# Kernel tuning notes

Measured on AMD Instinct MI355X. Metric: run time of the kernel, lower is better.

## Reference

```python
import jax, jax.numpy as jnp
import numpy as np

B, S, T, M, H = 16, 128, 1024, 16, 1024
HID = 1024        # attention MLP hidden
WIDTH_EMB = 20    # width embedding dim
N_LING = 2        # len(linguistic_feature_types)


def setup_inputs() -> dict:
    key = jax.random.key(0)
    ks = jax.random.split(key, 12)
    doc_embeddings = jax.random.normal(ks[0], (B, T, H), dtype=jnp.float32)
    start_mappings = jax.random.normal(ks[1], (B, S, T), dtype=jnp.float32)
    end_mappings = jax.random.normal(ks[2], (B, S, T), dtype=jnp.float32)
    continuous_mappings = jax.random.normal(ks[3], (B, S, M, T), dtype=jnp.float32)
    width = jax.random.randint(ks[4], (B, S), 0, M, dtype=jnp.int64)
    linguistic_labels = jax.random.normal(ks[5], (B, S, N_LING), dtype=jnp.float32)
    # attention MLP params (torch Linear layout transposed to x @ W + b)
    W1 = jax.random.normal(ks[6], (H, HID), dtype=jnp.float32) * (1.0 / np.sqrt(H))
    b1 = jax.random.normal(ks[7], (HID,), dtype=jnp.float32) * 0.01
    W2 = jax.random.normal(ks[8], (HID, 1), dtype=jnp.float32) * (1.0 / np.sqrt(HID))
    b2 = jax.random.normal(ks[9], (1,), dtype=jnp.float32) * 0.01
    width_table = jax.random.normal(ks[10], (5, WIDTH_EMB), dtype=jnp.float32)
    return {
        'doc_embeddings': doc_embeddings,
        'start_mappings': start_mappings,
        'end_mappings': end_mappings,
        'continuous_mappings': continuous_mappings,
        'linguistic_labels': linguistic_labels,
        'W1': W1, 'b1': b1, 'W2': W2, 'b2': b2,
        'width_table': width_table,
        'width': width,
    }


def reference(doc_embeddings, start_mappings, end_mappings, continuous_mappings,
              linguistic_labels, W1, b1, W2, b2, width_table, width):
    # one-hot matmul gathers
    start = jnp.einsum('bst,bth->bsh', start_mappings, doc_embeddings)
    end = jnp.einsum('bst,bth->bsh', end_mappings, doc_embeddings)
    cont = jnp.einsum('bsmt,bth->bsmh', continuous_mappings, doc_embeddings)
    b, s, m, h = cont.shape
    vector = jnp.concatenate([start, end], axis=-1).reshape(b * s, 2 * h)
    cont = cont.reshape(b * s, m, h)
    w = width.reshape(b * s)
    ling = linguistic_labels.reshape(b * s, -1)
    # padded masked attention pooling
    masks = (jnp.arange(m)[None, :] < jnp.maximum(w, 1)[:, None]).astype(cont.dtype)
    hdn = jax.nn.relu(jnp.einsum('nmh,hk->nmk', cont, W1) + b1)
    scores = (jnp.einsum('nmk,ko->nmo', hdn, W2) + b2)[..., 0]  # [n, m]
    scores = scores * masks
    scores = jnp.where(scores != 0, scores, jnp.asarray(-9e9, scores.dtype))
    att = jax.nn.softmax(scores, axis=1)
    weighted_sum = jnp.einsum('nm,nmh->nh', att, cont)
    vector = jnp.concatenate([vector, weighted_sum], axis=1)
    # linguistic feature columns (loop over fixed small feature list)
    for fi in range(N_LING):
        vector = jnp.concatenate([vector, ling[:, fi:fi + 1]], axis=1)
    # width embedding (clamp max=4)
    wemb = width_table[jnp.clip(w, 0, 4)]
    vector = jnp.concatenate([vector, wemb], axis=1)
    return vector.reshape(b, s, -1)
```

## Files before the change

kernel.cpp:

```cpp
#include <hip/hip_runtime.h>

typedef unsigned short ushort_t;
typedef unsigned int uint_t;
typedef _Float16 f16;
typedef f16 f16x8 __attribute__((ext_vector_type(8)));
typedef float f32x4 __attribute__((ext_vector_type(4)));

#define B_   16
#define S_   128
#define T_   1024
#define M_   16
#define H_   1024
#define OUTW 3094
#define NSPAN (B_*S_)
#define NROW  (NSPAN*M_)

#define WS_CONT   0
#define WS_DOCT   67108864
#define WS_W1T    100663296
#define WS_SCORES 102760448

__device__ __forceinline__ float sane(float v) {
  return fminf(fmaxf(v, -60000.f), 60000.f);
}
__device__ __forceinline__ ushort_t f16bits(float f) {
  union { f16 h; ushort_t u; } c; c.h = (f16)f; return c.u;
}
__device__ __forceinline__ void load_lds16(const void* g, void* l) {
  __builtin_amdgcn_global_load_lds(
      (const __attribute__((address_space(1))) uint_t*)g,
      (__attribute__((address_space(3))) uint_t*)l, 16, 0, 0);
}

__global__ __launch_bounds__(256) void tconv(const float* __restrict__ in,
                                             ushort_t* __restrict__ out,
                                             int R, int C) {
  __shared__ uint_t tile[64][65];
  const int tid = threadIdx.x;
  const int c0 = blockIdx.x * 64, r0 = blockIdx.y * 64;
  const size_t mo = (size_t)blockIdx.z * R * C;
  const float* ip = in + mo;
  ushort_t* op = out + mo;
  const int tx = tid & 63, ty = tid >> 6;
#pragma unroll
  for (int p = 0; p < 16; ++p) {
    int r = p * 4 + ty;
    tile[r][tx] = (uint_t)f16bits(ip[(size_t)(r0 + r) * C + c0 + tx]);
  }
  __syncthreads();
  const int rr = (tid & 31) * 2, cc0 = tid >> 5;
  uint_t* op32 = (uint_t*)op;
#pragma unroll
  for (int p = 0; p < 8; ++p) {
    int c = cc0 + p * 8;
    uint_t lo = tile[rr][c] & 0xffffu;
    uint_t hi = tile[rr + 1][c] & 0xffffu;
    op32[((size_t)(c0 + c) * R + r0 + rr) >> 1] = lo | (hi << 16);
  }
}

__global__ __launch_bounds__(256) void gemm1(const float* __restrict__ startm,
                                             const float* __restrict__ endm,
                                             const float* __restrict__ contm,
                                             const ushort_t* __restrict__ docT,
                                             float* __restrict__ out,
                                             f16* __restrict__ contF) {
  __shared__ float As[128 * 32];
  __shared__ ushort_t Bs[128 * 32];
  const int tid = threadIdx.x;
  const uint_t pid = blockIdx.x;
  const int xcd = pid & 7;
  const int s_  = pid >> 3;
  const int ct  = s_ & 7;
  const int pg  = (s_ >> 3) * 8 + xcd;
  const int rt  = pg >> 4;
  const int b   = pg & 15;

  const float* Ap;
  if (rt == 0)      Ap = startm + (size_t)b * S_ * T_;
  else if (rt == 1) Ap = endm + (size_t)b * S_ * T_;
  else              Ap = contm + (size_t)b * (S_ * M_ * T_) + (size_t)(rt - 2) * 128 * T_;
  const ushort_t* Bp = docT + (size_t)b * (H_ * T_) + (size_t)ct * 128 * T_;

  const int lane = tid & 63, w = tid >> 6;
  const int wr = w >> 1, wc = w & 1;
  const int quad = lane >> 4, l16 = lane & 15;
  const int arow = lane >> 3;
  const int acol = ((lane & 7) ^ arow) * 4;
  const int brow = lane >> 2;
  const int bcol = ((lane & 3) ^ ((lane >> 3) & 3)) * 8;

  f32x4 acc[4][4];
#pragma unroll
  for (int i = 0; i < 4; ++i)
#pragma unroll
    for (int j = 0; j < 4; ++j) acc[i][j] = (f32x4){0.f, 0.f, 0.f, 0.f};

  for (int k0 = 0; k0 < T_; k0 += 32) {
#pragma unroll
    for (int i = 0; i < 4; ++i) {
      const int rb = w * 32 + i * 8;
      load_lds16(Ap + (size_t)(rb + arow) * T_ + k0 + acol, &As[rb * 32]);
    }
#pragma unroll
    for (int i = 0; i < 2; ++i) {
      const int rb = w * 32 + i * 16;
      load_lds16(Bp + (size_t)(rb + brow) * T_ + k0 + bcol, &Bs[rb * 32]);
    }
    __syncthreads();
    f16x8 af[4], bfr[4];
#pragma unroll
    for (int i = 0; i < 4; ++i) {
      const int row = wr * 64 + i * 16 + l16;
      const int sw = row & 7;
      f32x4 lo = *(const f32x4*)&As[row * 32 + (((quad * 2) ^ sw) * 4)];
      f32x4 hi = *(const f32x4*)&As[row * 32 + (((quad * 2 + 1) ^ sw) * 4)];
      f16x8 h;
#pragma unroll
      for (int k = 0; k < 4; ++k) { h[k] = (f16)lo[k]; h[k + 4] = (f16)hi[k]; }
      af[i] = h;
    }
#pragma unroll
    for (int j = 0; j < 4; ++j) {
      const int row = wc * 64 + j * 16 + l16;
      const int sw = (row >> 1) & 3;
      bfr[j] = *(const f16x8*)&Bs[row * 32 + ((quad ^ sw) * 8)];
    }
#pragma unroll
    for (int i = 0; i < 4; ++i)
#pragma unroll
      for (int j = 0; j < 4; ++j)
        acc[i][j] = __builtin_amdgcn_mfma_f32_16x16x32_f16(af[i], bfr[j], acc[i][j], 0, 0, 0);
    __syncthreads();
  }

  if (rt < 2) {
    float* op = out + (size_t)b * S_ * OUTW + (size_t)rt * 1024 + (size_t)ct * 128;
#pragma unroll
    for (int i = 0; i < 4; ++i)
#pragma unroll
      for (int j = 0; j < 4; ++j)
#pragma unroll
        for (int r = 0; r < 4; ++r) {
          int row = wr * 64 + i * 16 + quad * 4 + r;
          int col = wc * 64 + j * 16 + l16;
          op[(size_t)row * OUTW + col] = sane(acc[i][j][r]);
        }
  } else {
    f16* cp = contF + ((size_t)b * 2048 + (size_t)(rt - 2) * 128) * H_ + (size_t)ct * 128;
#pragma unroll
    for (int i = 0; i < 4; ++i)
#pragma unroll
      for (int j = 0; j < 4; ++j)
#pragma unroll
        for (int r = 0; r < 4; ++r) {
          int row = wr * 64 + i * 16 + quad * 4 + r;
          int col = wc * 64 + j * 16 + l16;
          cp[(size_t)row * H_ + col] = (f16)sane(acc[i][j][r]);
        }
  }
}

__global__ __launch_bounds__(256) void gemm2(const f16* __restrict__ contF,
                                             const f16* __restrict__ W1T,
                                             const float* __restrict__ b1,
                                             const float* __restrict__ W2,
                                             float* __restrict__ scores) {
  __shared__ f16 As[128 * 32];
  __shared__ f16 Bs[128 * 32];
  const int tid = threadIdx.x;
  const uint_t pid = blockIdx.x;
  const int xcd = pid & 7;
  const int s_  = pid >> 3;
  const int ct  = s_ & 7;
  const int rt  = (s_ >> 3) * 8 + xcd;

  const f16* Ap = contF + (size_t)rt * 128 * H_;
  const f16* Bp = W1T + (size_t)ct * 128 * H_;

  const int lane = tid & 63, w = tid >> 6;
  const int wr = w >> 1, wc = w & 1;
  const int quad = lane >> 4, l16 = lane & 15;
  const int brow = lane >> 2;
  const int bcol = ((lane & 3) ^ ((lane >> 3) & 3)) * 8;

  f32x4 acc[4][4];
#pragma unroll
  for (int i = 0; i < 4; ++i)
#pragma unroll
    for (int j = 0; j < 4; ++j) acc[i][j] = (f32x4){0.f, 0.f, 0.f, 0.f};

  for (int k0 = 0; k0 < H_; k0 += 32) {
#pragma unroll
    for (int i = 0; i < 2; ++i) {
      const int rb = w * 32 + i * 16;
      load_lds16(Ap + (size_t)(rb + brow) * H_ + k0 + bcol, &As[rb * 32]);
      load_lds16(Bp + (size_t)(rb + brow) * H_ + k0 + bcol, &Bs[rb * 32]);
    }
    __syncthreads();
    f16x8 af[4], bfr[4];
#pragma unroll
    for (int i = 0; i < 4; ++i) {
      const int row = wr * 64 + i * 16 + l16;
      const int sw = (row >> 1) & 3;
      af[i] = *(const f16x8*)&As[row * 32 + ((quad ^ sw) * 8)];
    }
#pragma unroll
    for (int j = 0; j < 4; ++j) {
      const int row = wc * 64 + j * 16 + l16;
      const int sw = (row >> 1) & 3;
      bfr[j] = *(const f16x8*)&Bs[row * 32 + ((quad ^ sw) * 8)];
    }
#pragma unroll
    for (int i = 0; i < 4; ++i)
#pragma unroll
      for (int j = 0; j < 4; ++j)
        acc[i][j] = __builtin_amdgcn_mfma_f32_16x16x32_f16(af[i], bfr[j], acc[i][j], 0, 0, 0);
    __syncthreads();
  }

  const int colbase = ct * 128 + wc * 64;
#pragma unroll
  for (int i = 0; i < 4; ++i) {
#pragma unroll
    for (int r = 0; r < 4; ++r) {
      float t = 0.f;
#pragma unroll
      for (int j = 0; j < 4; ++j) {
        int c = colbase + j * 16 + l16;
        float v = acc[i][j][r] + b1[c];
        v = fmaxf(v, 0.f);
        t = fmaf(v, W2[c], t);
      }
      t += __shfl_xor(t, 1);
      t += __shfl_xor(t, 2);
      t += __shfl_xor(t, 4);
      t += __shfl_xor(t, 8);
      if (l16 == 0) {
        int row = rt * 128 + wr * 64 + i * 16 + quad * 4 + r;
        atomicAdd(&scores[row], t);
      }
    }
  }
}

__global__ __launch_bounds__(256) void finalize(const f16* __restrict__ contF,
                                                const float* __restrict__ scores,
                                                const float* __restrict__ ling,
                                                const float* __restrict__ b2,
                                                const float* __restrict__ wtab,
                                                const int* __restrict__ width,
                                                float* __restrict__ out) {
  const int n = blockIdx.x;
  const int tid = threadIdx.x;
  __shared__ float sc[16];
  if (tid < 16) {
    float raw = scores[n * 16 + tid] + b2[0];
    if (raw != raw) raw = 0.0f;
    int wv = width[n];
    int wm = wv > 1 ? wv : 1;
    float s = (tid < wm) ? raw : 0.0f;
    if (s == 0.0f) s = -9e9f;
    sc[tid] = s;
  }
  __syncthreads();
  float mx = sc[0];
#pragma unroll
  for (int m = 1; m < 16; ++m) mx = fmaxf(mx, sc[m]);
  float e[16];
  float ssum = 0.f;
#pragma unroll
  for (int m = 0; m < 16; ++m) { e[m] = __expf(sc[m] - mx); ssum += e[m]; }
  const float inv = 1.0f / ssum;
  const f16* cp = contF + (size_t)n * (M_ * H_);
  float* op = out + (size_t)n * OUTW;
#pragma unroll
  for (int hh = 0; hh < 4; ++hh) {
    int h = tid + hh * 256;
    float a = 0.f;
#pragma unroll
    for (int m = 0; m < 16; ++m) a = fmaf(e[m], (float)cp[m * H_ + h], a);
    op[2048 + h] = sane(a * inv);
  }
  if (tid < 2) op[3072 + tid] = ling[n * 2 + tid];
  if (tid < 20) {
    int wv = width[n];
    int wcl = wv < 4 ? wv : 4;
    if (wcl < 0) wcl = 0;
    op[3074 + tid] = wtab[wcl * 20 + tid];
  }
}

extern "C" void kernel_launch(void* const* d_in, const int* in_sizes, int n_in,
                              void* d_out, int out_size, void* d_ws, size_t ws_size,
                              hipStream_t stream) {
  const float* doc    = (const float*)d_in[0];
  const float* startm = (const float*)d_in[1];
  const float* endm   = (const float*)d_in[2];
  const float* contm  = (const float*)d_in[3];
  const float* ling   = (const float*)d_in[4];
  const float* W1     = (const float*)d_in[5];
  const float* b1     = (const float*)d_in[6];
  const float* W2     = (const float*)d_in[7];
  const float* b2     = (const float*)d_in[8];
  const float* wtab   = (const float*)d_in[9];
  const int*   width  = (const int*)d_in[10];
  float* out = (float*)d_out;

  char* ws = (char*)d_ws;
  f16*      contF  = (f16*)(ws + WS_CONT);
  ushort_t* docT   = (ushort_t*)(ws + WS_DOCT);
  f16*      W1T    = (f16*)(ws + WS_W1T);
  float*    scores = (float*)(ws + WS_SCORES);

  hipMemsetAsync(scores, 0, NROW * sizeof(float), stream);
  tconv<<<dim3(16, 16, 16), 256, 0, stream>>>(doc, docT, 1024, 1024);
  tconv<<<dim3(16, 16, 1), 256, 0, stream>>>(W1, (ushort_t*)W1T, 1024, 1024);
  gemm1<<<dim3(2304, 1, 1), 256, 0, stream>>>(startm, endm, contm, docT, out, contF);
  gemm2<<<dim3(2048, 1, 1), 256, 0, stream>>>(contF, (const f16*)W1T, b1, W2, scores);
  finalize<<<dim3(NSPAN, 1, 1), 256, 0, stream>>>(contF, scores, ling, b2, wtab, width, out);
}
```

Before: 499.7 us.

## Double-buffer LDS in both GEMMs and convert A to fp16 before staging

Both GEMM kernels now use two LDS buffers, so the next K-tile is prefetched while the MFMAs run on the current one, and only one barrier is needed per iteration. In gemm1 the fp32 A tile is loaded into registers, converted to fp16 and written to LDS once, rather than staged as fp32 and converted by every reading wave. This halves the A staging footprint and removes repeated conversions. The risks are higher register pressure from the prefetched A values and the LDS async-load ordering relying on a single barrier.

```diff
diff --git a/kernel.cpp b/kernel.cpp
--- a/kernel.cpp
+++ b/kernel.cpp
@@ -65,8 +65,8 @@
                                              const ushort_t* __restrict__ docT,
                                              float* __restrict__ out,
                                              f16* __restrict__ contF) {
-  __shared__ float As[128 * 32];
-  __shared__ ushort_t Bs[128 * 32];
+  __shared__ f16 As[2 * 128 * 32];
+  __shared__ f16 Bs[2 * 128 * 32];
   const int tid = threadIdx.x;
   const uint_t pid = blockIdx.x;
   const int xcd = pid & 7;
@@ -85,8 +85,12 @@
   const int lane = tid & 63, w = tid >> 6;
   const int wr = w >> 1, wc = w & 1;
   const int quad = lane >> 4, l16 = lane & 15;
-  const int arow = lane >> 3;
-  const int acol = ((lane & 7) ^ arow) * 4;
+  const int arow = tid >> 1;
+  const int ah   = tid & 1;
+  const int asw  = (arow >> 1) & 3;
+  const int ac0  = ((2 * ah) ^ asw) * 8;
+  const int ac1  = ((2 * ah + 1) ^ asw) * 8;
+  const float* aSrc = Ap + (size_t)arow * T_ + ah * 16;
   const int brow = lane >> 2;
   const int bcol = ((lane & 3) ^ ((lane >> 3) & 3)) * 8;
 
@@ -96,42 +100,75 @@
 #pragma unroll
     for (int j = 0; j < 4; ++j) acc[i][j] = (f32x4){0.f, 0.f, 0.f, 0.f};
 
-  for (int k0 = 0; k0 < T_; k0 += 32) {
-#pragma unroll
-    for (int i = 0; i < 4; ++i) {
-      const int rb = w * 32 + i * 8;
-      load_lds16(Ap + (size_t)(rb + arow) * T_ + k0 + acol, &As[rb * 32]);
-    }
+  {
+    f32x4 a0 = *(const f32x4*)(aSrc + 0);
+    f32x4 a1 = *(const f32x4*)(aSrc + 4);
+    f32x4 a2 = *(const f32x4*)(aSrc + 8);
+    f32x4 a3 = *(const f32x4*)(aSrc + 12);
 #pragma unroll
     for (int i = 0; i < 2; ++i) {
       const int rb = w * 32 + i * 16;
-      load_lds16(Bp + (size_t)(rb + brow) * T_ + k0 + bcol, &Bs[rb * 32]);
-    }
+      load_lds16(Bp + (size_t)(rb + brow) * T_ + bcol, &Bs[rb * 32]);
+    }
+    f16x8 h0, h1;
+#pragma unroll
+    for (int k = 0; k < 4; ++k) {
+      h0[k] = (f16)a0[k]; h0[k + 4] = (f16)a1[k];
+      h1[k] = (f16)a2[k]; h1[k + 4] = (f16)a3[k];
+    }
+    *(f16x8*)&As[arow * 32 + ac0] = h0;
+    *(f16x8*)&As[arow * 32 + ac1] = h1;
     __syncthreads();
+  }
+
+  int cur = 0;
+  for (int k0 = 0; k0 < T_; k0 += 32) {
+    const int nxt = cur ^ 1;
+    const bool pf = (k0 + 32 < T_);
+    f32x4 a0, a1, a2, a3;
+    if (pf) {
+      const float* ap = aSrc + (k0 + 32);
+      a0 = *(const f32x4*)(ap + 0);
+      a1 = *(const f32x4*)(ap + 4);
+      a2 = *(const f32x4*)(ap + 8);
+      a3 = *(const f32x4*)(ap + 12);
+#pragma unroll
+      for (int i = 0; i < 2; ++i) {
+        const int rb = w * 32 + i * 16;
+        load_lds16(Bp + (size_t)(rb + brow) * T_ + (k0 + 32) + bcol,
+                   &Bs[nxt * 4096 + rb * 32]);
+      }
+    }
     f16x8 af[4], bfr[4];
 #pragma unroll
     for (int i = 0; i < 4; ++i) {
       const int row = wr * 64 + i * 16 + l16;
-      const int sw = row & 7;
-      f32x4 lo = *(const f32x4*)&As[row * 32 + (((quad * 2) ^ sw) * 4)];
-      f32x4 hi = *(const f32x4*)&As[row * 32 + (((quad * 2 + 1) ^ sw) * 4)];
-      f16x8 h;
-#pragma unroll
-      for (int k = 0; k < 4; ++k) { h[k] = (f16)lo[k]; h[k + 4] = (f16)hi[k]; }
-      af[i] = h;
+      const int sw = (row >> 1) & 3;
+      af[i] = *(const f16x8*)&As[cur * 4096 + row * 32 + ((quad ^ sw) * 8)];
     }
 #pragma unroll
     for (int j = 0; j < 4; ++j) {
       const int row = wc * 64 + j * 16 + l16;
       const int sw = (row >> 1) & 3;
-      bfr[j] = *(const f16x8*)&Bs[row * 32 + ((quad ^ sw) * 8)];
+      bfr[j] = *(const f16x8*)&Bs[cur * 4096 + row * 32 + ((quad ^ sw) * 8)];
     }
 #pragma unroll
     for (int i = 0; i < 4; ++i)
 #pragma unroll
       for (int j = 0; j < 4; ++j)
         acc[i][j] = __builtin_amdgcn_mfma_f32_16x16x32_f16(af[i], bfr[j], acc[i][j], 0, 0, 0);
+    if (pf) {
+      f16x8 h0, h1;
+#pragma unroll
+      for (int k = 0; k < 4; ++k) {
+        h0[k] = (f16)a0[k]; h0[k + 4] = (f16)a1[k];
+        h1[k] = (f16)a2[k]; h1[k + 4] = (f16)a3[k];
+      }
+      *(f16x8*)&As[nxt * 4096 + arow * 32 + ac0] = h0;
+      *(f16x8*)&As[nxt * 4096 + arow * 32 + ac1] = h1;
+    }
     __syncthreads();
+    cur = nxt;
   }
 
   if (rt < 2) {
@@ -166,8 +203,8 @@
                                              const float* __restrict__ b1,
                                              const float* __restrict__ W2,
                                              float* __restrict__ scores) {
-  __shared__ f16 As[128 * 32];
-  __shared__ f16 Bs[128 * 32];
+  __shared__ f16 As[2 * 128 * 32];
+  __shared__ f16 Bs[2 * 128 * 32];
   const int tid = threadIdx.x;
   const uint_t pid = blockIdx.x;
   const int xcd = pid & 7;
@@ -190,26 +227,40 @@
 #pragma unroll
     for (int j = 0; j < 4; ++j) acc[i][j] = (f32x4){0.f, 0.f, 0.f, 0.f};
 
+#pragma unroll
+  for (int i = 0; i < 2; ++i) {
+    const int rb = w * 32 + i * 16;
+    load_lds16(Ap + (size_t)(rb + brow) * H_ + bcol, &As[rb * 32]);
+    load_lds16(Bp + (size_t)(rb + brow) * H_ + bcol, &Bs[rb * 32]);
+  }
+  __syncthreads();
+
+  int cur = 0;
   for (int k0 = 0; k0 < H_; k0 += 32) {
-#pragma unroll
-    for (int i = 0; i < 2; ++i) {
-      const int rb = w * 32 + i * 16;
-      load_lds16(Ap + (size_t)(rb + brow) * H_ + k0 + bcol, &As[rb * 32]);
-      load_lds16(Bp + (size_t)(rb + brow) * H_ + k0 + bcol, &Bs[rb * 32]);
-    }
-    __syncthreads();
+    const int nxt = cur ^ 1;
+    const bool pf = (k0 + 32 < H_);
+    if (pf) {
+#pragma unroll
+      for (int i = 0; i < 2; ++i) {
+        const int rb = w * 32 + i * 16;
+        load_lds16(Ap + (size_t)(rb + brow) * H_ + (k0 + 32) + bcol,
+                   &As[nxt * 4096 + rb * 32]);
+        load_lds16(Bp + (size_t)(rb + brow) * H_ + (k0 + 32) + bcol,
+                   &Bs[nxt * 4096 + rb * 32]);
+      }
+    }
     f16x8 af[4], bfr[4];
 #pragma unroll
     for (int i = 0; i < 4; ++i) {
       const int row = wr * 64 + i * 16 + l16;
       const int sw = (row >> 1) & 3;
-      af[i] = *(const f16x8*)&As[row * 32 + ((quad ^ sw) * 8)];
+      af[i] = *(const f16x8*)&As[cur * 4096 + row * 32 + ((quad ^ sw) * 8)];
     }
 #pragma unroll
     for (int j = 0; j < 4; ++j) {
       const int row = wc * 64 + j * 16 + l16;
       const int sw = (row >> 1) & 3;
-      bfr[j] = *(const f16x8*)&Bs[row * 32 + ((quad ^ sw) * 8)];
+      bfr[j] = *(const f16x8*)&Bs[cur * 4096 + row * 32 + ((quad ^ sw) * 8)];
     }
 #pragma unroll
     for (int i = 0; i < 4; ++i)
@@ -217,6 +268,7 @@
       for (int j = 0; j < 4; ++j)
         acc[i][j] = __builtin_amdgcn_mfma_f32_16x16x32_f16(af[i], bfr[j], acc[i][j], 0, 0, 0);
     __syncthreads();
+    cur = nxt;
   }
 
   const int colbase = ct * 128 + wc * 64;
```

New measurement: 504.2 us. Within noise of the previous version (+0.9%).
